# Kernel tuning notes

Measured on AMD Instinct MI355X. Metric: run time of the kernel, lower is better.

The kernel has to match this reference:

```python
import jax, jax.numpy as jnp
import numpy as np

B, L, D, H = 48, 512, 192, 6
DK = D // H
HID = 4 * D
EPS = 1e-5
SCALE = 1.0 / np.float32(np.sqrt(DK))


def _ln(x, g, b):
    mu = x.mean(-1, keepdims=True)
    v = ((x - mu) ** 2).mean(-1, keepdims=True)
    return (x - mu) * jax.lax.rsqrt(v + EPS) * g + b


def _mln(x, m, g, b):
    # masked layernorm: valid rows normalized, invalid rows pass through unchanged
    return jnp.where(m[..., None], _ln(x, g, b), x)


def _mha(q, k, v, mask, wq, bq, wk, bk, wv, bv, wo, bo):
    def proj(x, w, bb):
        return (x @ w + bb).reshape(B, L, H, DK).transpose(0, 2, 1, 3)  # [B,H,L,dk]
    Q, K, V = proj(q, wq, bq), proj(k, wk, bk), proj(v, wv, bv)
    s = jnp.einsum('bhqd,bhkd->bhqk', Q, K) * SCALE
    s = jnp.where(mask[:, None], -1e9, s)  # mask True = invalid pair
    p = jax.nn.softmax(s, axis=-1)
    o = jnp.einsum('bhqk,bhkd->bhqd', p, V).transpose(0, 2, 1, 3).reshape(B, L, D)
    return o @ wo + bo


def _forward(x_a, x_b, valid_a, valid_b,
             ln_a_g, ln_a_b, ln_b_g, ln_b_b, ln_oa_g, ln_oa_b, ln_ob_g, ln_ob_b,
             wq, bq, wk, bk, wv, bv, wo, bo,
             fln_g, fln_b, flno_g, flno_b, w1, b1, w2, b2):
    mB2A = ~(valid_a[:, :, None] & valid_b[:, None, :])  # [B,La,Lb]
    mA2B = ~(valid_b[:, :, None] & valid_a[:, None, :])
    a = _mln(x_a, valid_a, ln_a_g, ln_a_b)
    b = _mln(x_b, valid_b, ln_b_g, ln_b_b)
    oa = _mha(a, b, b, mB2A, wq, bq, wk, bk, wv, bv, wo, bo)
    oa = _mln(oa + x_a, valid_a, ln_oa_g, ln_oa_b)
    ob = _mha(b, a, a, mA2B, wq, bq, wk, bk, wv, bv, wo, bo)
    ob = _mln(ob + x_b, valid_b, ln_ob_g, ln_ob_b)

    def ffn(x, m):
        xn = _mln(x, m, fln_g, fln_b)
        y = jax.nn.gelu(xn @ w1 + b1, approximate=False) @ w2 + b2
        return _mln(x + y, m, flno_g, flno_b)

    return ffn(oa, valid_a), ffn(ob, valid_b)


def setup_inputs() -> dict:
    key = jax.random.key(0)
    ks = jax.random.split(key, 12)
    p = lambda k, s: jax.random.normal(k, s, dtype=jnp.float32) * 0.02
    ones = lambda s: jnp.ones(s, dtype=jnp.float32)
    zeros = lambda s: jnp.zeros(s, dtype=jnp.float32)
    return {
        'x_a': jax.random.normal(ks[0], (B, L, D), dtype=jnp.float32),
        'x_b': jax.random.normal(ks[1], (B, L, D), dtype=jnp.float32),
        'valid_a': jax.random.bernoulli(ks[2], 0.9, (B, L)),
        'valid_b': jax.random.bernoulli(ks[3], 0.9, (B, L)),
        'ln_a_g': ones((D,)), 'ln_a_b': zeros((D,)),
        'ln_b_g': ones((D,)), 'ln_b_b': zeros((D,)),
        'ln_oa_g': ones((D,)), 'ln_oa_b': zeros((D,)),
        'ln_ob_g': ones((D,)), 'ln_ob_b': zeros((D,)),
        'wq': p(ks[4], (D, D)), 'bq': zeros((D,)),
        'wk': p(ks[5], (D, D)), 'bk': zeros((D,)),
        'wv': p(ks[6], (D, D)), 'bv': zeros((D,)),
        'wo': p(ks[7], (D, D)), 'bo': zeros((D,)),
        'fln_g': ones((D,)), 'fln_b': zeros((D,)),
        'flno_g': ones((D,)), 'flno_b': zeros((D,)),
        'w1': p(ks[8], (D, HID)), 'b1': zeros((HID,)),
        'w2': p(ks[9], (HID, D)), 'b2': zeros((D,)),
    }


def reference(x_a, x_b, valid_a, valid_b,
              ln_a_g, ln_a_b, ln_b_g, ln_b_b, ln_oa_g, ln_oa_b, ln_ob_g, ln_ob_b,
              wq, bq, wk, bk, wv, bv, wo, bo,
              fln_g, fln_b, flno_g, flno_b, w1, b1, w2, b2):
    return _forward(x_a, x_b, valid_a, valid_b,
                    ln_a_g, ln_a_b, ln_b_g, ln_b_b, ln_oa_g, ln_oa_b, ln_ob_g, ln_ob_b,
                    wq, bq, wk, bk, wv, bv, wo, bo,
                    fln_g, fln_b, flno_g, flno_b, w1, b1, w2, b2)
```

## Files before the change

### kernel.cpp

```cpp
#include <hip/hip_runtime.h>
#include <math.h>

#define BB 48
#define LL 512
#define DD 192
#define HH 6
#define DKK 32
#define HID 768
#define ROWS (BB * LL)
#define BLD ((size_t)ROWS * DD)
#define SB2 0.25503531f
#define MASKED_X (-36.0f)

typedef unsigned short ushort_t;
typedef unsigned int uint_t;
typedef __bf16 bf16x8 __attribute__((ext_vector_type(8)));
typedef float f32x4 __attribute__((ext_vector_type(4)));

union U4BF8 { uint4 u; bf16x8 b; };
union BFU { __bf16 h; ushort_t u; };

__device__ __forceinline__ ushort_t f2bf(float f) {
  union { float f; uint_t u; } v; v.f = f;
  uint_t r = v.u + 0x7fffu + ((v.u >> 16) & 1u);
  return (ushort_t)(r >> 16);
}
__device__ __forceinline__ ushort_t cvt_bf(float f) {
  BFU c; c.h = (__bf16)f; return c.u;
}

__device__ __forceinline__ int swz_w(int n, int k, int N) {
  return ((k >> 5) * (N >> 4) + (n >> 4)) * 512 +
         ((((k & 31) >> 3) << 4) + (n & 15)) * 8 + (k & 7);
}

__global__ __launch_bounds__(256) void pack_kernel(
    const float* __restrict__ wq, const float* __restrict__ wk,
    const float* __restrict__ wv, const float* __restrict__ wo,
    const float* __restrict__ w1, const float* __restrict__ w2,
    const float* __restrict__ bq, const float* __restrict__ bk,
    const float* __restrict__ bv,
    ushort_t* __restrict__ Wqkv, ushort_t* __restrict__ Wo,
    ushort_t* __restrict__ W1, ushort_t* __restrict__ W2,
    float* __restrict__ bqkv) {
  int i = blockIdx.x * 256 + threadIdx.x;
  if (i < 110592) {
    int n2 = i / 192, k = i - n2 * 192;
    int part = n2 / 192, n = n2 - part * 192;
    const float* src = part == 0 ? wq : (part == 1 ? wk : wv);
    Wqkv[swz_w(n2, k, 576)] = f2bf(src[k * 192 + n]);
  } else if (i < 147456) {
    int j = i - 110592;
    int n = j / 192, k = j - n * 192;
    Wo[swz_w(n, k, 192)] = f2bf(wo[k * 192 + n]);
  } else if (i < 294912) {
    int j = i - 147456;
    int n = j / 192, k = j - n * 192;
    W1[j] = f2bf(w1[k * 768 + n]);
  } else if (i < 442368) {
    int j = i - 294912;
    int n = j / 768, k = j - n * 768;
    W2[j] = f2bf(w2[k * 192 + n]);
  } else if (i < 442944) {
    int j = i - 442368;
    bqkv[j] = j < 192 ? bq[j] : (j < 384 ? bk[j - 192] : bv[j - 384]);
  }
}

__global__ __launch_bounds__(256) void qkv_ln_kernel(
    const float* __restrict__ xa, const float* __restrict__ xb,
    const int* __restrict__ va, const int* __restrict__ vb,
    const float* __restrict__ g_a, const float* __restrict__ b_a,
    const float* __restrict__ g_b, const float* __restrict__ b_b,
    const ushort_t* __restrict__ Wsw, const float* __restrict__ bias,
    ushort_t* __restrict__ Cb) {
  constexpr int N = 576;
  constexpr int CSB = N + 8;
  __shared__ ushort_t smem[32 * CSB];
  ushort_t* As = smem;

  int tid = threadIdx.x;
  int w = tid >> 6, lane = tid & 63, l15 = lane & 15, kq = lane >> 4;
  int row0 = blockIdx.x * 32;
  int side = row0 >= ROWS;
  int rb = row0 - side * ROWS;

  {
    int row = tid >> 3, l8 = tid & 7;
    const float* xr = (side ? xb : xa) + (size_t)(rb + row) * DD + l8 * 24;
    float v[24];
    float s = 0.f;
#pragma unroll
    for (int j = 0; j < 6; ++j) {
      float4 q = *(const float4*)(xr + j * 4);
      v[j*4+0] = q.x; v[j*4+1] = q.y; v[j*4+2] = q.z; v[j*4+3] = q.w;
      s += q.x + q.y + q.z + q.w;
    }
    s += __shfl_xor(s, 1); s += __shfl_xor(s, 2); s += __shfl_xor(s, 4);
    float mu = s * (1.0f / 192.0f);
    float ss = 0.f;
#pragma unroll
    for (int j = 0; j < 24; ++j) { float d = v[j] - mu; ss += d * d; }
    ss += __shfl_xor(ss, 1); ss += __shfl_xor(ss, 2); ss += __shfl_xor(ss, 4);
    float inv = rsqrtf(ss * (1.0f / 192.0f) + 1e-5f);
    int vld = (side ? vb : va)[rb + row];
    const float* g = side ? g_b : g_a;
    const float* be = side ? b_b : b_a;
    ushort_t ob[24];
#pragma unroll
    for (int j = 0; j < 24; ++j) {
      int col = l8 * 24 + j;
      float r = vld ? (v[j] - mu) * inv * g[col] + be[col] : v[j];
      ob[j] = f2bf(r);
    }
#pragma unroll
    for (int j = 0; j < 3; ++j)
      *(uint4*)(&As[row * 200 + l8 * 24 + j * 8]) = *(const uint4*)(&ob[j * 8]);
  }
  __syncthreads();

  f32x4 acc[2][9];
#pragma unroll
  for (int qs = 0; qs < 2; ++qs)
#pragma unroll
    for (int nt = 0; nt < 9; ++nt) acc[qs][nt] = (f32x4){0.f, 0.f, 0.f, 0.f};

#pragma unroll 1
  for (int kk = 0; kk < 6; ++kk) {
    bf16x8 af[2];
#pragma unroll
    for (int qs = 0; qs < 2; ++qs)
      af[qs] = *(const bf16x8*)(&As[(qs * 16 + l15) * 200 + kk * 32 + kq * 8]);
    const ushort_t* wp =
        Wsw + ((size_t)(kk * (N >> 4) + w * 9) << 9) + lane * 8;
#pragma unroll
    for (int nt = 0; nt < 9; ++nt) {
      U4BF8 wf;
      wf.u = *(const uint4*)(wp + (nt << 9));
#pragma unroll
      for (int qs = 0; qs < 2; ++qs)
        acc[qs][nt] = __builtin_amdgcn_mfma_f32_16x16x32_bf16(
            af[qs], wf.b, acc[qs][nt], 0, 0, 0);
    }
  }
  __syncthreads();

  ushort_t* Cs = smem;
#pragma unroll
  for (int nt = 0; nt < 9; ++nt) {
    int col = (w * 9 + nt) * 16 + l15;
    float bb = bias[col];
#pragma unroll
    for (int qs = 0; qs < 2; ++qs)
#pragma unroll
      for (int r = 0; r < 4; ++r)
        Cs[(qs * 16 + kq * 4 + r) * CSB + col] = f2bf(acc[qs][nt][r] + bb);
  }
  __syncthreads();
  constexpr int UPR = (N * 2) / 16;
#pragma unroll
  for (int i = 0; i < (32 * UPR) / 256; ++i) {
    int idx = tid + i * 256;
    int r = idx / UPR, u = idx - r * UPR;
    *(uint4*)(Cb + (size_t)row0 * N + idx * 8) =
        *(const uint4*)(&Cs[r * CSB + u * 8]);
  }
}

__global__ __launch_bounds__(256) void oproj_ln_kernel(
    const ushort_t* __restrict__ A, const ushort_t* __restrict__ Wsw,
    const float* __restrict__ bias,
    const float* __restrict__ xa, const float* __restrict__ xb,
    const int* __restrict__ va, const int* __restrict__ vb,
    const float* __restrict__ g_oa, const float* __restrict__ b_oa,
    const float* __restrict__ g_ob, const float* __restrict__ b_ob,
    const float* __restrict__ g_f, const float* __restrict__ b_f,
    float* __restrict__ outf, ushort_t* __restrict__ outb) {
  __shared__ float smemf[32 * 196];
  ushort_t* As = (ushort_t*)smemf;

  int tid = threadIdx.x;
  int w = tid >> 6, lane = tid & 63, l15 = lane & 15, kq = lane >> 4;
  int row0 = blockIdx.x * 32;
  int side = row0 >= ROWS;
  int rb = row0 - side * ROWS;

  {
    const ushort_t* ap = A + (size_t)row0 * DD;
#pragma unroll
    for (int i = 0; i < 3; ++i) {
      int idx = tid + i * 256;
      int r = idx / 24, c = (idx - r * 24) * 8;
      *(uint4*)(&As[r * 200 + c]) = *(const uint4*)(ap + idx * 8);
    }
  }
  __syncthreads();

  f32x4 acc[2][3];
#pragma unroll
  for (int qs = 0; qs < 2; ++qs)
#pragma unroll
    for (int nt = 0; nt < 3; ++nt) acc[qs][nt] = (f32x4){0.f, 0.f, 0.f, 0.f};

#pragma unroll 1
  for (int kk = 0; kk < 6; ++kk) {
    bf16x8 af[2];
#pragma unroll
    for (int qs = 0; qs < 2; ++qs)
      af[qs] = *(const bf16x8*)(&As[(qs * 16 + l15) * 200 + kk * 32 + kq * 8]);
    const ushort_t* wp =
        Wsw + ((size_t)(kk * (192 >> 4) + w * 3) << 9) + lane * 8;
#pragma unroll
    for (int nt = 0; nt < 3; ++nt) {
      U4BF8 wf;
      wf.u = *(const uint4*)(wp + (nt << 9));
#pragma unroll
      for (int qs = 0; qs < 2; ++qs)
        acc[qs][nt] = __builtin_amdgcn_mfma_f32_16x16x32_bf16(
            af[qs], wf.b, acc[qs][nt], 0, 0, 0);
    }
  }
  __syncthreads();

  float* Cs = smemf;
#pragma unroll
  for (int nt = 0; nt < 3; ++nt) {
    int col = (w * 3 + nt) * 16 + l15;
    float bb = bias[col];
#pragma unroll
    for (int qs = 0; qs < 2; ++qs)
#pragma unroll
      for (int r = 0; r < 4; ++r)
        Cs[(qs * 16 + kq * 4 + r) * 196 + col] = acc[qs][nt][r] + bb;
  }
  __syncthreads();

  int row = tid >> 3, l8 = tid & 7;
  int grow = row0 + row;
  const float* resr = (side ? xb : xa) + (size_t)(rb + row) * DD + l8 * 24;
  const float* cr = &Cs[row * 196 + l8 * 24];
  float v[24];
  float s = 0.f;
#pragma unroll
  for (int j = 0; j < 6; ++j) {
    float4 q = *(const float4*)(resr + j * 4);
    v[j*4+0] = cr[j*4+0] + q.x; v[j*4+1] = cr[j*4+1] + q.y;
    v[j*4+2] = cr[j*4+2] + q.z; v[j*4+3] = cr[j*4+3] + q.w;
    s += v[j*4+0] + v[j*4+1] + v[j*4+2] + v[j*4+3];
  }
  s += __shfl_xor(s, 1); s += __shfl_xor(s, 2); s += __shfl_xor(s, 4);
  float mu = s * (1.0f / 192.0f);
  float ss = 0.f;
#pragma unroll
  for (int j = 0; j < 24; ++j) { float d = v[j] - mu; ss += d * d; }
  ss += __shfl_xor(ss, 1); ss += __shfl_xor(ss, 2); ss += __shfl_xor(ss, 4);
  float inv = rsqrtf(ss * (1.0f / 192.0f) + 1e-5f);
  int vld = (side ? vb : va)[rb + row];
  const float* g1 = side ? g_ob : g_oa;
  const float* b1 = side ? b_ob : b_oa;
  float y[24];
#pragma unroll
  for (int j = 0; j < 24; ++j) {
    int col = l8 * 24 + j;
    y[j] = vld ? (v[j] - mu) * inv * g1[col] + b1[col] : v[j];
  }
  float* op = outf + (size_t)grow * DD + l8 * 24;
#pragma unroll
  for (int j = 0; j < 6; ++j) {
    float4 q = {y[j*4+0], y[j*4+1], y[j*4+2], y[j*4+3]};
    *(float4*)(op + j * 4) = q;
  }
  float s2 = 0.f;
#pragma unroll
  for (int j = 0; j < 24; ++j) s2 += y[j];
  s2 += __shfl_xor(s2, 1); s2 += __shfl_xor(s2, 2); s2 += __shfl_xor(s2, 4);
  float mu2 = s2 * (1.0f / 192.0f);
  float ss2 = 0.f;
#pragma unroll
  for (int j = 0; j < 24; ++j) { float e = y[j] - mu2; ss2 += e * e; }
  ss2 += __shfl_xor(ss2, 1); ss2 += __shfl_xor(ss2, 2); ss2 += __shfl_xor(ss2, 4);
  float inv2 = rsqrtf(ss2 * (1.0f / 192.0f) + 1e-5f);
  ushort_t zb[24];
#pragma unroll
  for (int j = 0; j < 24; ++j) {
    int col = l8 * 24 + j;
    float z = vld ? (y[j] - mu2) * inv2 * g_f[col] + b_f[col] : y[j];
    zb[j] = f2bf(z);
  }
  ushort_t* ob = outb + (size_t)grow * DD + l8 * 24;
#pragma unroll
  for (int j = 0; j < 3; ++j)
    *(uint4*)(ob + j * 8) = *(const uint4*)(&zb[j * 8]);
}

__global__ __launch_bounds__(256, 3) void ffn_fused_kernel(
    const ushort_t* __restrict__ A, const ushort_t* __restrict__ W1t,
    const float* __restrict__ bias1, const ushort_t* __restrict__ W2t,
    const float* __restrict__ bias2,
    const int* __restrict__ va, const int* __restrict__ vb,
    const float* __restrict__ g_f, const float* __restrict__ b_f,
    float* __restrict__ outf) {
  __shared__ float smemf[64 * 196];
  ushort_t* As = (ushort_t*)smemf;
  ushort_t* Hs = As + 64 * 200;

  int tid = threadIdx.x;
  int w = tid >> 6;
  int lane = tid & 63;
  int l15 = lane & 15;
  int kq = lane >> 4;
  int row0 = blockIdx.x * 64;
  int side = row0 >= ROWS;
  int rb0 = row0 - side * ROWS;

#pragma unroll
  for (int i = 0; i < 6; ++i) {
    int idx = tid + i * 256;
    int r = idx / 24, c = (idx % 24) * 8;
    *(uint4*)(&As[r * 200 + c]) = *(const uint4*)(A + (size_t)(row0 + r) * DD + c);
  }

  const ushort_t* w1p = W1t + (size_t)(w * 16 + l15) * DD + kq * 8;
  const ushort_t* w2p = W2t + (size_t)(w * 48 + l15) * HID + kq * 8;

  U4BF8 w1f[6], w1n[6], w2f[6];
#pragma unroll
  for (int kk = 0; kk < 6; ++kk)
    w1f[kk].u = *(const uint4*)(w1p + kk * 32);

  f32x4 Cacc[4][3];
#pragma unroll
  for (int qs = 0; qs < 4; ++qs)
#pragma unroll
    for (int nt = 0; nt < 3; ++nt) Cacc[qs][nt] = (f32x4){0.f, 0.f, 0.f, 0.f};

  __syncthreads();

  for (int hc = 0; hc < 12; ++hc) {
#pragma unroll
    for (int kk2 = 0; kk2 < 2; ++kk2)
#pragma unroll
      for (int nt = 0; nt < 3; ++nt)
        w2f[kk2 * 3 + nt].u =
            *(const uint4*)(w2p + (size_t)(nt * 16) * HID + hc * 64 + kk2 * 32);

    f32x4 Hacc[4];
#pragma unroll
    for (int qs = 0; qs < 4; ++qs) Hacc[qs] = (f32x4){0.f, 0.f, 0.f, 0.f};
#pragma unroll
    for (int kk = 0; kk < 6; ++kk) {
#pragma unroll
      for (int qs = 0; qs < 4; ++qs) {
        bf16x8 af = *(const bf16x8*)(&As[(qs * 16 + l15) * 200 + kk * 32 + kq * 8]);
        Hacc[qs] = __builtin_amdgcn_mfma_f32_16x16x32_bf16(
            af, w1f[kk].b, Hacc[qs], 0, 0, 0);
      }
    }

    if (hc < 11) {
#pragma unroll
      for (int kk = 0; kk < 6; ++kk)
        w1n[kk].u = *(const uint4*)(w1p + (size_t)(hc + 1) * 64 * DD + kk * 32);
    }

    {
      float bb = bias1[hc * 64 + w * 16 + l15];
      ushort_t* hb = &Hs[(hc & 1) * 4608];
#pragma unroll
      for (int qs = 0; qs < 4; ++qs)
#pragma unroll
        for (int r = 0; r < 4; ++r) {
          float x = Hacc[qs][r] + bb;
          x = 0.5f * x * (1.0f + erff(x * 0.70710678118654752f));
          hb[(qs * 16 + kq * 4 + r) * 72 + w * 16 + l15] = f2bf(x);
        }
    }
    __syncthreads();

#pragma unroll
    for (int kk2 = 0; kk2 < 2; ++kk2) {
      bf16x8 hf[4];
#pragma unroll
      for (int qs = 0; qs < 4; ++qs)
        hf[qs] = *(const bf16x8*)(&Hs[(hc & 1) * 4608 +
                                      (qs * 16 + l15) * 72 + kk2 * 32 + kq * 8]);
#pragma unroll
      for (int nt = 0; nt < 3; ++nt)
#pragma unroll
        for (int qs = 0; qs < 4; ++qs)
          Cacc[qs][nt] = __builtin_amdgcn_mfma_f32_16x16x32_bf16(
              hf[qs], w2f[kk2 * 3 + nt].b, Cacc[qs][nt], 0, 0, 0);
    }

#pragma unroll
    for (int kk = 0; kk < 6; ++kk) w1f[kk] = w1n[kk];
  }
  __syncthreads();

  float* Cs = smemf;
#pragma unroll
  for (int qs = 0; qs < 4; ++qs)
#pragma unroll
    for (int nt = 0; nt < 3; ++nt) {
      int col = w * 48 + nt * 16 + l15;
      float bb = bias2[col];
#pragma unroll
      for (int r = 0; r < 4; ++r)
        Cs[(qs * 16 + kq * 4 + r) * 196 + col] = Cacc[qs][nt][r] + bb;
    }
  __syncthreads();

  int row = tid >> 2, l4 = tid & 3;
  int grow = row0 + row;
  float* op = outf + (size_t)grow * DD + l4 * 48;
  const float* cr = &Cs[row * 196 + l4 * 48];
  float v[48];
  float s = 0.f;
#pragma unroll
  for (int j = 0; j < 12; ++j) {
    float4 q = *(const float4*)(op + j * 4);
    v[j*4+0] = cr[j*4+0] + q.x; v[j*4+1] = cr[j*4+1] + q.y;
    v[j*4+2] = cr[j*4+2] + q.z; v[j*4+3] = cr[j*4+3] + q.w;
    s += v[j*4+0] + v[j*4+1] + v[j*4+2] + v[j*4+3];
  }
  s += __shfl_xor(s, 1); s += __shfl_xor(s, 2);
  float mu = s * (1.0f / 192.0f);
  float ss = 0.f;
#pragma unroll
  for (int j = 0; j < 48; ++j) { float d = v[j] - mu; ss += d * d; }
  ss += __shfl_xor(ss, 1); ss += __shfl_xor(ss, 2);
  float inv = rsqrtf(ss * (1.0f / 192.0f) + 1e-5f);
  int vld = (side ? vb : va)[rb0 + row];
#pragma unroll
  for (int j = 0; j < 12; ++j) {
    float4 q;
    float* vv = &v[j * 4];
#pragma unroll
    for (int e = 0; e < 4; ++e) {
      int col = l4 * 48 + j * 4 + e;
      ((float*)&q)[e] = vld ? (vv[e] - mu) * inv * g_f[col] + b_f[col] : vv[e];
    }
    *(float4*)(op + j * 4) = q;
  }
}

__global__ __launch_bounds__(256) void attn_mfma_kernel(
    const ushort_t* __restrict__ QKV,
    const int* __restrict__ valid_a, const int* __restrict__ valid_b,
    ushort_t* __restrict__ out) {
  int i = blockIdx.x;
  int gid = ((i >> 5) << 3) | (i & 7);
  int qt = (i >> 3) & 3;
  int side = gid >= BB * HH;
  int grem = side ? gid - BB * HH : gid;
  int h = grem % HH;
  int batch = grem / HH;
  int tid = threadIdx.x;
  int w = tid >> 6;
  int lane = tid & 63;
  int l15 = lane & 15;
  int kq = lane >> 4;

  const int* validq = side ? valid_b : valid_a;
  const int* validk = side ? valid_a : valid_b;
  size_t qrow0  = (size_t)side * ROWS + (size_t)batch * LL;
  size_t kvrow0 = (size_t)(1 - side) * ROWS + (size_t)batch * LL;

  __shared__ ushort_t VsT[2][32 * 72];
  __shared__ ushort_t Ps[4][32 * 72];

  int qbase = qt * 128 + w * 32;

  U4BF8 qfrag[2];
#pragma unroll
  for (int qs = 0; qs < 2; ++qs)
    qfrag[qs].u = *(const uint4*)(QKV + (qrow0 + qbase + qs * 16 + l15) * 576 +
                                  h * DKK + kq * 8);

  float sqf[2][4], mq[2][4];
#pragma unroll
  for (int qs = 0; qs < 2; ++qs)
#pragma unroll
    for (int r = 0; r < 4; ++r) {
      int vq = validq[batch * LL + qbase + qs * 16 + kq * 4 + r];
      sqf[qs][r] = vq ? SB2 : 0.0f;
      mq[qs][r]  = vq ? 0.0f : MASKED_X;
    }

  float lsum[2][4];
  f32x4 Oacc[2][2];
#pragma unroll
  for (int qs = 0; qs < 2; ++qs) {
#pragma unroll
    for (int r = 0; r < 4; ++r) lsum[qs][r] = 0.0f;
#pragma unroll
    for (int ds = 0; ds < 2; ++ds) Oacc[qs][ds] = (f32x4){0.f, 0.f, 0.f, 0.f};
  }

  uint4 vv = *(const uint4*)(QKV + (kvrow0 + lane) * 576 + 384 + h * DKK + w * 8);
  U4BF8 kf[4];
  int vki[4];
#pragma unroll
  for (int ks = 0; ks < 4; ++ks) {
    kf[ks].u = *(const uint4*)(QKV + (kvrow0 + ks * 16 + l15) * 576 +
                               192 + h * DKK + kq * 8);
    vki[ks] = validk[batch * LL + ks * 16 + l15];
  }

  for (int c = 0; c < LL; c += 64) {
    int buf = (c >> 6) & 1;
    {
      uint_t uu[4] = {vv.x, vv.y, vv.z, vv.w};
#pragma unroll
      for (int j = 0; j < 4; ++j) {
        VsT[buf][(w * 8 + 2 * j) * 72 + lane]     = (ushort_t)(uu[j] & 0xffffu);
        VsT[buf][(w * 8 + 2 * j + 1) * 72 + lane] = (ushort_t)(uu[j] >> 16);
      }
    }
    uint4 vvn;
    if (c + 64 < LL)
      vvn = *(const uint4*)(QKV + (kvrow0 + c + 64 + lane) * 576 +
                            384 + h * DKK + w * 8);
    __syncthreads();

    f32x4 S[2][4];
#pragma unroll
    for (int ks = 0; ks < 4; ++ks)
#pragma unroll
      for (int qs = 0; qs < 2; ++qs) {
        f32x4 z = (f32x4){0.f, 0.f, 0.f, 0.f};
        S[qs][ks] = __builtin_amdgcn_mfma_f32_16x16x32_bf16(
            qfrag[qs].b, kf[ks].b, z, 0, 0, 0);
      }

    float mkb[4];
#pragma unroll
    for (int ks = 0; ks < 4; ++ks) mkb[ks] = vki[ks] ? 0.0f : MASKED_X;

    U4BF8 kfn[4];
    int vkn[4];
    if (c + 64 < LL) {
#pragma unroll
      for (int ks = 0; ks < 4; ++ks) {
        kfn[ks].u = *(const uint4*)(QKV + (kvrow0 + c + 64 + ks * 16 + l15) * 576 +
                                    192 + h * DKK + kq * 8);
        vkn[ks] = validk[batch * LL + c + 64 + ks * 16 + l15];
      }
    }

#pragma unroll
    for (int qs = 0; qs < 2; ++qs)
#pragma unroll
      for (int ks = 0; ks < 4; ++ks)
#pragma unroll
        for (int r = 0; r < 4; ++r) {
          float xs = fmaf(S[qs][ks][r], sqf[qs][r], fminf(mq[qs][r], mkb[ks]));
          float p = __builtin_amdgcn_exp2f(xs);
          lsum[qs][r] += p;
          Ps[w][(qs * 16 + kq * 4 + r) * 72 + ks * 16 + l15] = cvt_bf(p);
        }

#pragma unroll
    for (int kh = 0; kh < 2; ++kh) {
      bf16x8 pf[2], vf[2];
#pragma unroll
      for (int qs = 0; qs < 2; ++qs)
        pf[qs] = *(const bf16x8*)(&Ps[w][(qs * 16 + l15) * 72 + kh * 32 + kq * 8]);
#pragma unroll
      for (int ds = 0; ds < 2; ++ds)
        vf[ds] = *(const bf16x8*)(&VsT[buf][(ds * 16 + l15) * 72 + kh * 32 + kq * 8]);
#pragma unroll
      for (int qs = 0; qs < 2; ++qs)
#pragma unroll
        for (int ds = 0; ds < 2; ++ds)
          Oacc[qs][ds] = __builtin_amdgcn_mfma_f32_16x16x32_bf16(
              pf[qs], vf[ds], Oacc[qs][ds], 0, 0, 0);
    }

    vv = vvn;
#pragma unroll
    for (int ks = 0; ks < 4; ++ks) { kf[ks] = kfn[ks]; vki[ks] = vkn[ks]; }
  }

#pragma unroll
  for (int qs = 0; qs < 2; ++qs)
#pragma unroll
    for (int r = 0; r < 4; ++r) {
      float sm = lsum[qs][r];
#pragma unroll
      for (int off = 1; off < 16; off <<= 1) sm += __shfl_xor(sm, off);
      lsum[qs][r] = sm;
    }

#pragma unroll
  for (int qs = 0; qs < 2; ++qs)
#pragma unroll
    for (int ds = 0; ds < 2; ++ds)
#pragma unroll
      for (int r = 0; r < 4; ++r) {
        int q = qbase + qs * 16 + kq * 4 + r;
        out[(qrow0 + q) * DD + h * DKK + ds * 16 + l15] =
            f2bf(Oacc[qs][ds][r] / lsum[qs][r]);
      }
}

extern "C" void kernel_launch(void* const* d_in, const int* in_sizes, int n_in,
                              void* d_out, int out_size, void* d_ws, size_t ws_size,
                              hipStream_t stream) {
  const float* x_a = (const float*)d_in[0];
  const float* x_b = (const float*)d_in[1];
  const int* valid_a = (const int*)d_in[2];
  const int* valid_b = (const int*)d_in[3];
  const float* ln_a_g = (const float*)d_in[4];
  const float* ln_a_b = (const float*)d_in[5];
  const float* ln_b_g = (const float*)d_in[6];
  const float* ln_b_b = (const float*)d_in[7];
  const float* ln_oa_g = (const float*)d_in[8];
  const float* ln_oa_b = (const float*)d_in[9];
  const float* ln_ob_g = (const float*)d_in[10];
  const float* ln_ob_b = (const float*)d_in[11];
  const float* wq = (const float*)d_in[12];
  const float* bq = (const float*)d_in[13];
  const float* wk = (const float*)d_in[14];
  const float* bk = (const float*)d_in[15];
  const float* wv = (const float*)d_in[16];
  const float* bv = (const float*)d_in[17];
  const float* wo = (const float*)d_in[18];
  const float* bo = (const float*)d_in[19];
  const float* fln_g = (const float*)d_in[20];
  const float* fln_b = (const float*)d_in[21];
  const float* flno_g = (const float*)d_in[22];
  const float* flno_b = (const float*)d_in[23];
  const float* w1 = (const float*)d_in[24];
  const float* b1 = (const float*)d_in[25];
  const float* w2 = (const float*)d_in[26];
  const float* b2 = (const float*)d_in[27];

  char* wsb = (char*)d_ws;
  ushort_t* Wqkv = (ushort_t*)wsb;
  ushort_t* Wo_t = Wqkv + 110592;
  ushort_t* W1_t = Wo_t + 36864;
  ushort_t* W2_t = W1_t + 147456;
  float*    bqkv = (float*)(W2_t + 147456);
  ushort_t* lnFull = (ushort_t*)(wsb + 887040);
  ushort_t* attO   = lnFull;
  ushort_t* QKV = (ushort_t*)(wsb + 19761408);

  float* out_a = (float*)d_out;

  dim3 b256(256);
  dim3 gGemm(2 * ROWS / 32);
  dim3 gAttn(BB * HH * 4 * 2);
  dim3 gFFN(2 * ROWS / 64);

  hipLaunchKernelGGL(pack_kernel, dim3(1731), b256, 0, stream,
                     wq, wk, wv, wo, w1, w2, bq, bk, bv,
                     Wqkv, Wo_t, W1_t, W2_t, bqkv);

  hipLaunchKernelGGL(qkv_ln_kernel, gGemm, b256, 0, stream,
                     x_a, x_b, valid_a, valid_b,
                     ln_a_g, ln_a_b, ln_b_g, ln_b_b,
                     Wqkv, bqkv, QKV);

  hipLaunchKernelGGL(attn_mfma_kernel, gAttn, b256, 0, stream,
                     QKV, valid_a, valid_b, attO);

  hipLaunchKernelGGL(oproj_ln_kernel, gGemm, b256, 0, stream,
                     attO, Wo_t, bo, x_a, x_b, valid_a, valid_b,
                     ln_oa_g, ln_oa_b, ln_ob_g, ln_ob_b, fln_g, fln_b,
                     out_a, lnFull);

  hipLaunchKernelGGL(ffn_fused_kernel, gFFN, b256, 0, stream,
                     lnFull, W1_t, b1, W2_t, b2, valid_a, valid_b,
                     flno_g, flno_b, out_a);
}
```

Baseline: 396.0 us.

## Interleave LayerNorm column mapping and drop attention K/V register prefetch

The two LayerNorm epilogues now give each thread strided 4-wide column chunks (j*32+l8*4 or j*16+l4*4) instead of one contiguous span per thread. Adjacent lanes therefore touch adjacent global and shared addresses, which should coalesce accesses and reduce LDS bank conflicts. The attention kernel drops its double-buffered V tile and register prefetch of the next K/V chunk, loading each chunk inside the loop with two barriers. This cuts register and LDS use, which may raise occupancy, but load latency is no longer hidden behind compute.

```diff
diff --git a/kernel.cpp b/kernel.cpp
--- a/kernel.cpp
+++ b/kernel.cpp
@@ -237,15 +237,16 @@
 
   int row = tid >> 3, l8 = tid & 7;
   int grow = row0 + row;
-  const float* resr = (side ? xb : xa) + (size_t)(rb + row) * DD + l8 * 24;
-  const float* cr = &Cs[row * 196 + l8 * 24];
+  const float* xrow = (side ? xb : xa) + (size_t)(rb + row) * DD;
+  const float* crow = &Cs[row * 196];
   float v[24];
   float s = 0.f;
 #pragma unroll
   for (int j = 0; j < 6; ++j) {
-    float4 q = *(const float4*)(resr + j * 4);
-    v[j*4+0] = cr[j*4+0] + q.x; v[j*4+1] = cr[j*4+1] + q.y;
-    v[j*4+2] = cr[j*4+2] + q.z; v[j*4+3] = cr[j*4+3] + q.w;
+    int col = j * 32 + l8 * 4;
+    float4 q = *(const float4*)(xrow + col);
+    v[j*4+0] = crow[col+0] + q.x; v[j*4+1] = crow[col+1] + q.y;
+    v[j*4+2] = crow[col+2] + q.z; v[j*4+3] = crow[col+3] + q.w;
     s += v[j*4+0] + v[j*4+1] + v[j*4+2] + v[j*4+3];
   }
   s += __shfl_xor(s, 1); s += __shfl_xor(s, 2); s += __shfl_xor(s, 4);
@@ -260,15 +261,19 @@
   const float* b1 = side ? b_ob : b_oa;
   float y[24];
 #pragma unroll
-  for (int j = 0; j < 24; ++j) {
-    int col = l8 * 24 + j;
-    y[j] = vld ? (v[j] - mu) * inv * g1[col] + b1[col] : v[j];
-  }
-  float* op = outf + (size_t)grow * DD + l8 * 24;
+  for (int j = 0; j < 6; ++j) {
+#pragma unroll
+    for (int e = 0; e < 4; ++e) {
+      int col = j * 32 + l8 * 4 + e;
+      float vv = v[j * 4 + e];
+      y[j * 4 + e] = vld ? (vv - mu) * inv * g1[col] + b1[col] : vv;
+    }
+  }
+  float* orow = outf + (size_t)grow * DD;
 #pragma unroll
   for (int j = 0; j < 6; ++j) {
     float4 q = {y[j*4+0], y[j*4+1], y[j*4+2], y[j*4+3]};
-    *(float4*)(op + j * 4) = q;
+    *(float4*)(orow + j * 32 + l8 * 4) = q;
   }
   float s2 = 0.f;
 #pragma unroll
@@ -280,17 +285,18 @@
   for (int j = 0; j < 24; ++j) { float e = y[j] - mu2; ss2 += e * e; }
   ss2 += __shfl_xor(ss2, 1); ss2 += __shfl_xor(ss2, 2); ss2 += __shfl_xor(ss2, 4);
   float inv2 = rsqrtf(ss2 * (1.0f / 192.0f) + 1e-5f);
-  ushort_t zb[24];
-#pragma unroll
-  for (int j = 0; j < 24; ++j) {
-    int col = l8 * 24 + j;
-    float z = vld ? (y[j] - mu2) * inv2 * g_f[col] + b_f[col] : y[j];
-    zb[j] = f2bf(z);
-  }
-  ushort_t* ob = outb + (size_t)grow * DD + l8 * 24;
-#pragma unroll
-  for (int j = 0; j < 3; ++j)
-    *(uint4*)(ob + j * 8) = *(const uint4*)(&zb[j * 8]);
+  ushort_t* obrow = outb + (size_t)grow * DD;
+#pragma unroll
+  for (int j = 0; j < 6; ++j) {
+    ushort_t zb[4];
+#pragma unroll
+    for (int e = 0; e < 4; ++e) {
+      int col = j * 32 + l8 * 4 + e;
+      float z = vld ? (y[j*4+e] - mu2) * inv2 * g_f[col] + b_f[col] : y[j*4+e];
+      zb[e] = f2bf(z);
+    }
+    *(uint2*)(obrow + j * 32 + l8 * 4) = *(const uint2*)(&zb[0]);
+  }
 }
 
 __global__ __launch_bounds__(256, 3) void ffn_fused_kernel(
@@ -412,15 +418,16 @@
 
   int row = tid >> 2, l4 = tid & 3;
   int grow = row0 + row;
-  float* op = outf + (size_t)grow * DD + l4 * 48;
-  const float* cr = &Cs[row * 196 + l4 * 48];
+  float* orow = outf + (size_t)grow * DD;
+  const float* crow = &Cs[row * 196];
   float v[48];
   float s = 0.f;
 #pragma unroll
   for (int j = 0; j < 12; ++j) {
-    float4 q = *(const float4*)(op + j * 4);
-    v[j*4+0] = cr[j*4+0] + q.x; v[j*4+1] = cr[j*4+1] + q.y;
-    v[j*4+2] = cr[j*4+2] + q.z; v[j*4+3] = cr[j*4+3] + q.w;
+    int col = j * 16 + l4 * 4;
+    float4 q = *(const float4*)(orow + col);
+    v[j*4+0] = crow[col+0] + q.x; v[j*4+1] = crow[col+1] + q.y;
+    v[j*4+2] = crow[col+2] + q.z; v[j*4+3] = crow[col+3] + q.w;
     s += v[j*4+0] + v[j*4+1] + v[j*4+2] + v[j*4+3];
   }
   s += __shfl_xor(s, 1); s += __shfl_xor(s, 2);
@@ -433,14 +440,14 @@
   int vld = (side ? vb : va)[rb0 + row];
 #pragma unroll
   for (int j = 0; j < 12; ++j) {
+    int col = j * 16 + l4 * 4;
     float4 q;
-    float* vv = &v[j * 4];
 #pragma unroll
     for (int e = 0; e < 4; ++e) {
-      int col = l4 * 48 + j * 4 + e;
-      ((float*)&q)[e] = vld ? (vv[e] - mu) * inv * g_f[col] + b_f[col] : vv[e];
-    }
-    *(float4*)(op + j * 4) = q;
+      float vv = v[j * 4 + e];
+      ((float*)&q)[e] = vld ? (vv - mu) * inv * g_f[col + e] + b_f[col + e] : vv;
+    }
+    *(float4*)(orow + col) = q;
   }
 }
 
@@ -466,7 +473,7 @@
   size_t qrow0  = (size_t)side * ROWS + (size_t)batch * LL;
   size_t kvrow0 = (size_t)(1 - side) * ROWS + (size_t)batch * LL;
 
-  __shared__ ushort_t VsT[2][32 * 72];
+  __shared__ ushort_t VsT[32 * 72];
   __shared__ ushort_t Ps[4][32 * 72];
 
   int qbase = qt * 128 + w * 32;
@@ -497,54 +504,31 @@
     for (int ds = 0; ds < 2; ++ds) Oacc[qs][ds] = (f32x4){0.f, 0.f, 0.f, 0.f};
   }
 
-  uint4 vv = *(const uint4*)(QKV + (kvrow0 + lane) * 576 + 384 + h * DKK + w * 8);
-  U4BF8 kf[4];
-  int vki[4];
-#pragma unroll
-  for (int ks = 0; ks < 4; ++ks) {
-    kf[ks].u = *(const uint4*)(QKV + (kvrow0 + ks * 16 + l15) * 576 +
-                               192 + h * DKK + kq * 8);
-    vki[ks] = validk[batch * LL + ks * 16 + l15];
-  }
-
   for (int c = 0; c < LL; c += 64) {
-    int buf = (c >> 6) & 1;
-    {
-      uint_t uu[4] = {vv.x, vv.y, vv.z, vv.w};
-#pragma unroll
-      for (int j = 0; j < 4; ++j) {
-        VsT[buf][(w * 8 + 2 * j) * 72 + lane]     = (ushort_t)(uu[j] & 0xffffu);
-        VsT[buf][(w * 8 + 2 * j + 1) * 72 + lane] = (ushort_t)(uu[j] >> 16);
-      }
-    }
-    uint4 vvn;
-    if (c + 64 < LL)
-      vvn = *(const uint4*)(QKV + (kvrow0 + c + 64 + lane) * 576 +
-                            384 + h * DKK + w * 8);
     __syncthreads();
+    uint4 vv = *(const uint4*)(QKV + (kvrow0 + c + lane) * 576 +
+                               384 + h * DKK + w * 8);
+    uint_t uu[4] = {vv.x, vv.y, vv.z, vv.w};
+#pragma unroll
+    for (int j = 0; j < 4; ++j) {
+      VsT[(w * 8 + 2 * j) * 72 + lane]     = (ushort_t)(uu[j] & 0xffffu);
+      VsT[(w * 8 + 2 * j + 1) * 72 + lane] = (ushort_t)(uu[j] >> 16);
+    }
+    __syncthreads();
 
     f32x4 S[2][4];
-#pragma unroll
-    for (int ks = 0; ks < 4; ++ks)
+    float mkb[4];
+#pragma unroll
+    for (int ks = 0; ks < 4; ++ks) {
+      U4BF8 kf;
+      kf.u = *(const uint4*)(QKV + (kvrow0 + c + ks * 16 + l15) * 576 +
+                             192 + h * DKK + kq * 8);
+      mkb[ks] = validk[batch * LL + c + ks * 16 + l15] ? 0.0f : MASKED_X;
 #pragma unroll
       for (int qs = 0; qs < 2; ++qs) {
         f32x4 z = (f32x4){0.f, 0.f, 0.f, 0.f};
         S[qs][ks] = __builtin_amdgcn_mfma_f32_16x16x32_bf16(
-            qfrag[qs].b, kf[ks].b, z, 0, 0, 0);
-      }
-
-    float mkb[4];
-#pragma unroll
-    for (int ks = 0; ks < 4; ++ks) mkb[ks] = vki[ks] ? 0.0f : MASKED_X;
-
-    U4BF8 kfn[4];
-    int vkn[4];
-    if (c + 64 < LL) {
-#pragma unroll
-      for (int ks = 0; ks < 4; ++ks) {
-        kfn[ks].u = *(const uint4*)(QKV + (kvrow0 + c + 64 + ks * 16 + l15) * 576 +
-                                    192 + h * DKK + kq * 8);
-        vkn[ks] = validk[batch * LL + c + 64 + ks * 16 + l15];
+            qfrag[qs].b, kf.b, z, 0, 0, 0);
       }
     }
 
@@ -568,7 +552,7 @@
         pf[qs] = *(const bf16x8*)(&Ps[w][(qs * 16 + l15) * 72 + kh * 32 + kq * 8]);
 #pragma unroll
       for (int ds = 0; ds < 2; ++ds)
-        vf[ds] = *(const bf16x8*)(&VsT[buf][(ds * 16 + l15) * 72 + kh * 32 + kq * 8]);
+        vf[ds] = *(const bf16x8*)(&VsT[(ds * 16 + l15) * 72 + kh * 32 + kq * 8]);
 #pragma unroll
       for (int qs = 0; qs < 2; ++qs)
 #pragma unroll
@@ -576,10 +560,6 @@
           Oacc[qs][ds] = __builtin_amdgcn_mfma_f32_16x16x32_bf16(
               pf[qs], vf[ds], Oacc[qs][ds], 0, 0, 0);
     }
-
-    vv = vvn;
-#pragma unroll
-    for (int ks = 0; ks < 4; ++ks) { kf[ks] = kfn[ks]; vki[ks] = vkn[ks]; }
   }
 
 #pragma unroll
```

Result: faster. 364.5 us (-8.0%).
